# Kernel optimization log

Measured on AMD Instinct MI355X. Metric: run time of the kernel, lower is better.

The kernel has to match this reference:

```python
import jax, jax.numpy as jnp
import numpy as np

B, S = 256, 32          # sequence layout for the final (b, s, 1) reshape
BATCH = B * S           # 8192 flattened rows processed per call
IN, U, OUT = 32, 128, 1 # sensory inputs, interneurons, motor outputs
UNFOLDS = 6             # semi-implicit ODE solver unfolds


def _syn_sigmoid(v, mu, sigma):
    # v: [B, P]; mu, sigma: [P, Q] -> [B, P, Q] per-synapse gate
    return jax.nn.sigmoid(sigma * (v[:, :, None] - mu))


def setup_inputs() -> dict:
    key = jax.random.key(0)
    ks = jax.random.split(key, 12)
    inputs = jax.random.normal(ks[0], (BATCH, IN), dtype=jnp.float32)
    state = jax.random.normal(ks[1], (BATCH, U), dtype=jnp.float32)
    # adjacency in {-1, 0, 1} (wiring polarity), baked into W / erev as in _get_variables
    sens_adj = jax.random.randint(ks[2], (IN, U), -1, 2).astype(jnp.float32)
    adj = jax.random.randint(ks[3], (U, U), -1, 2).astype(jnp.float32)
    sensory_mu = jax.random.uniform(ks[4], (IN, U)) * 0.5 + 0.3
    sensory_sigma = jax.random.uniform(ks[5], (IN, U)) * 5.0 + 3.0
    # NOTE: original applies +w_init_min OUTSIDE the |adj| mask; reproduced faithfully
    sensory_W = jnp.abs(sens_adj) * jax.random.uniform(ks[6], (IN, U)) * 0.9 + 0.1
    sensory_erev = sens_adj  # erev_init_factor = 1
    mu = jax.random.uniform(ks[7], (U, U)) * 0.5 + 0.3
    sigma = jax.random.uniform(ks[8], (U, U)) * 5.0 + 3.0
    W = jnp.abs(adj) * jax.random.uniform(ks[9], (U, U)) * 0.9 + 0.1
    erev = adj
    vleak = jax.random.uniform(ks[10], (U,)) * 0.4 - 0.2
    gleak = jnp.ones((U,), jnp.float32)        # gleak_init_min == gleak_init_max == 1
    cm_t = jnp.ones((U,), jnp.float32) * 0.5    # cm_init_min == cm_init_max == 0.5
    in_w = jnp.ones((IN,), jnp.float32)         # affine input mapping (init ones/zeros)
    in_b = jnp.zeros((IN,), jnp.float32)
    out_w = jnp.ones((OUT,), jnp.float32)       # affine output mapping
    out_b = jnp.zeros((OUT,), jnp.float32)
    return dict(inputs=inputs, state=state, sensory_mu=sensory_mu,
                sensory_sigma=sensory_sigma, sensory_W=sensory_W,
                sensory_erev=sensory_erev, mu=mu, sigma=sigma, W=W, erev=erev,
                vleak=vleak, gleak=gleak, cm_t=cm_t, in_w=in_w, in_b=in_b,
                out_w=out_w, out_b=out_b, b=B, s=S)


def reference(inputs, state, sensory_mu, sensory_sigma, sensory_W, sensory_erev,
              mu, sigma, W, erev, vleak, gleak, cm_t, in_w, in_b, out_w, out_b,
              b, s):
    x = inputs * in_w + in_b                                   # _map_inputs (Affine)
    # sensory synapse activations, computed once: [BATCH, IN, U]
    sa = sensory_W * _syn_sigmoid(x, sensory_mu, sensory_sigma)
    w_num_s = jnp.sum(sa * sensory_erev, axis=1)               # [BATCH, U]
    w_den_s = jnp.sum(sa, axis=1)                              # [BATCH, U]

    def step(v, _):
        wa = W * _syn_sigmoid(v, mu, sigma)                    # [BATCH, U, U]
        w_num = jnp.sum(wa * erev, axis=1) + w_num_s
        w_den = jnp.sum(wa, axis=1) + w_den_s
        v_new = (cm_t * v + gleak * vleak + w_num) / (cm_t + gleak + w_den)
        return v_new, None

    v, _ = jax.lax.scan(step, state, None, length=UNFOLDS)
    outputs = (v[:, :OUT] * out_w + out_b).reshape(b, s, 1)    # _map_outputs
    return outputs, v
```

## Files before the change

### kernel.cpp

```cpp
#include <hip/hip_runtime.h>

#define NIN 32
#define NU  128
#define RPB 8
#define RPT 4
#define UNFOLDS 6
#define LOG2E 1.44269504088896340736f

typedef float float4v __attribute__((ext_vector_type(4)));

#define SPN (NIN * NU)
#define RPN (NU * NU)

__global__ void pack_params(const float* __restrict__ mu,
                            const float* __restrict__ sig,
                            const float* __restrict__ W,
                            const float* __restrict__ erev,
                            float4v* __restrict__ out, int n) {
    int idx = blockIdx.x * blockDim.x + threadIdx.x;
    if (idx < n) {
        float sg = sig[idx];
        float s2 = -LOG2E * sg;
        float sm2 = -s2 * mu[idx];
        float Wv = W[idx];
        float We = Wv * erev[idx];
        out[idx] = (float4v){s2, sm2, We, Wv};
    }
}

template <bool PACKED>
__global__ __launch_bounds__(256, 4)
void wormnet_main(const float* __restrict__ inputs,
                  const float* __restrict__ state,
                  const float4v* __restrict__ sp,
                  const float4v* __restrict__ rp,
                  const float* __restrict__ smu, const float* __restrict__ ssig,
                  const float* __restrict__ sW,  const float* __restrict__ serev,
                  const float* __restrict__ rmu, const float* __restrict__ rsig,
                  const float* __restrict__ rW,  const float* __restrict__ rerev,
                  const float* __restrict__ vleak,
                  const float* __restrict__ gleak,
                  const float* __restrict__ cm_t,
                  const float* __restrict__ in_w, const float* __restrict__ in_b,
                  const float* __restrict__ out_w, const float* __restrict__ out_b,
                  float* __restrict__ out_y,
                  float* __restrict__ out_v)
{
    __shared__ __align__(16) float xs[NIN * RPB];
    __shared__ __align__(16) float vs[2][NU * RPB];

    const int tid  = threadIdx.x;
    const int j    = tid & (NU - 1);
    const int rh   = tid >> 7;
    const int r0   = rh * RPT;
    const int base = blockIdx.x * RPB;

    {
        int i = tid & (NIN - 1);
        int r = tid >> 5;
        xs[i * RPB + r] = inputs[(base + r) * NIN + i] * in_w[i] + in_b[i];
    }
    {
        #pragma unroll
        for (int k = 0; k < 4; ++k) {
            int r = rh + 2 * k;
            vs[0][j * RPB + r] = state[(base + r) * NU + j];
        }
    }
    __syncthreads();

    float numS[RPT], denS[RPT];
    #pragma unroll
    for (int r = 0; r < RPT; ++r) { numS[r] = 0.0f; denS[r] = 0.0f; }

    #pragma unroll 4
    for (int i = 0; i < NIN; ++i) {
        float4v p;
        if (PACKED) {
            p = sp[i * NU + j];
        } else {
            int idx = i * NU + j;
            float sg = ssig[idx];
            float s2 = -LOG2E * sg;
            p = (float4v){s2, -s2 * smu[idx], sW[idx] * serev[idx], sW[idx]};
        }
        float4v xv = *(const float4v*)&xs[i * RPB + r0];
        #pragma unroll
        for (int r = 0; r < RPT; ++r) {
            float t = __builtin_fmaf(p.x, xv[r], p.y);
            float e = __builtin_amdgcn_exp2f(t);
            float sgm = __builtin_amdgcn_rcpf(1.0f + e);
            numS[r] = __builtin_fmaf(p.z, sgm, numS[r]);
            denS[r] = __builtin_fmaf(p.w, sgm, denS[r]);
        }
    }

    const float cm = cm_t[j];
    const float gl = gleak[j];
    const float glvl = gl * vleak[j];
    const float cg = cm + gl;
    float vold[RPT];
    #pragma unroll
    for (int r = 0; r < RPT; ++r) vold[r] = vs[0][j * RPB + r0 + r];

    int cur = 0;
    for (int u = 0; u < UNFOLDS; ++u) {
        float num[RPT], den[RPT];
        #pragma unroll
        for (int r = 0; r < RPT; ++r) { num[r] = numS[r]; den[r] = denS[r]; }

        #pragma unroll 4
        for (int i = 0; i < NU; ++i) {
            float4v p;
            if (PACKED) {
                p = rp[i * NU + j];
            } else {
                int idx = i * NU + j;
                float sg = rsig[idx];
                float s2 = -LOG2E * sg;
                p = (float4v){s2, -s2 * rmu[idx], rW[idx] * rerev[idx], rW[idx]};
            }
            float4v vv = *(const float4v*)&vs[cur][i * RPB + r0];
            #pragma unroll
            for (int r = 0; r < RPT; ++r) {
                float t = __builtin_fmaf(p.x, vv[r], p.y);
                float e = __builtin_amdgcn_exp2f(t);
                float sgm = __builtin_amdgcn_rcpf(1.0f + e);
                num[r] = __builtin_fmaf(p.z, sgm, num[r]);
                den[r] = __builtin_fmaf(p.w, sgm, den[r]);
            }
        }

        float4v vnew;
        #pragma unroll
        for (int r = 0; r < RPT; ++r) {
            float tn = __builtin_fmaf(cm, vold[r], glvl) + num[r];
            float td = cg + den[r];
            float vn = tn * __builtin_amdgcn_rcpf(td);
            vold[r] = vn;
            vnew[r] = vn;
        }
        *(float4v*)&vs[cur ^ 1][j * RPB + r0] = vnew;
        __syncthreads();
        cur ^= 1;
    }

    #pragma unroll
    for (int r = 0; r < RPT; ++r) {
        out_v[(base + r0 + r) * NU + j] = vold[r];
    }
    if (j == 0) {
        const float ow = out_w[0], ob = out_b[0];
        #pragma unroll
        for (int r = 0; r < RPT; ++r) {
            out_y[base + r0 + r] = __builtin_fmaf(vold[r], ow, ob);
        }
    }
}

extern "C" void kernel_launch(void* const* d_in, const int* in_sizes, int n_in,
                              void* d_out, int out_size, void* d_ws, size_t ws_size,
                              hipStream_t stream) {
    const float* inputs  = (const float*)d_in[0];
    const float* state   = (const float*)d_in[1];
    const float* smu     = (const float*)d_in[2];
    const float* ssig    = (const float*)d_in[3];
    const float* sW      = (const float*)d_in[4];
    const float* serev   = (const float*)d_in[5];
    const float* rmu     = (const float*)d_in[6];
    const float* rsig    = (const float*)d_in[7];
    const float* rW      = (const float*)d_in[8];
    const float* rerev   = (const float*)d_in[9];
    const float* vleak   = (const float*)d_in[10];
    const float* gleak   = (const float*)d_in[11];
    const float* cm_t    = (const float*)d_in[12];
    const float* in_w    = (const float*)d_in[13];
    const float* in_b    = (const float*)d_in[14];
    const float* out_w   = (const float*)d_in[15];
    const float* out_b   = (const float*)d_in[16];

    const int batch = in_sizes[1] / NU;
    float* out_y = (float*)d_out;
    float* out_v = (float*)d_out + batch;

    const size_t need = (size_t)(SPN + RPN) * sizeof(float4v);
    const bool packed = ws_size >= need;
    float4v* sp = (float4v*)d_ws;
    float4v* rp = sp + SPN;

    if (packed) {
        hipLaunchKernelGGL(pack_params, dim3((SPN + 255) / 256), dim3(256), 0, stream,
                           smu, ssig, sW, serev, sp, SPN);
        hipLaunchKernelGGL(pack_params, dim3((RPN + 255) / 256), dim3(256), 0, stream,
                           rmu, rsig, rW, rerev, rp, RPN);
    }

    dim3 grid(batch / RPB), block(256);
    if (packed) {
        hipLaunchKernelGGL((wormnet_main<true>), grid, block, 0, stream,
                           inputs, state, sp, rp,
                           smu, ssig, sW, serev, rmu, rsig, rW, rerev,
                           vleak, gleak, cm_t, in_w, in_b, out_w, out_b,
                           out_y, out_v);
    } else {
        hipLaunchKernelGGL((wormnet_main<false>), grid, block, 0, stream,
                           inputs, state, sp, rp,
                           smu, ssig, sW, serev, rmu, rsig, rW, rerev,
                           vleak, gleak, cm_t, in_w, in_b, out_w, out_b,
                           out_y, out_v);
    }
}
```

Measured before the change: 277.8 us.

## Double rows per thread and pair sigmoid reciprocals to halve rcp count

Each block now handles 16 rows and each thread 8 rows, so every packed parameter load is reused across twice as many batch rows. Sigmoids are computed in pairs: one reciprocal of the product of two denominators gives both values, trading a transcendental rcp for extra multiplies. The unpacked fallback path is removed, so the kernel now assumes the workspace is large enough. Occupancy is lowered to 2 blocks per CU to make room for the larger register footprint, and the grid is halved.

```diff
diff --git a/kernel.cpp b/kernel.cpp
--- a/kernel.cpp
+++ b/kernel.cpp
@@ -2,8 +2,8 @@
 
 #define NIN 32
 #define NU  128
-#define RPB 8
-#define RPT 4
+#define RPB 16
+#define RPT 8
 #define UNFOLDS 6
 #define LOG2E 1.44269504088896340736f
 
@@ -28,16 +28,11 @@
     }
 }
 
-template <bool PACKED>
-__global__ __launch_bounds__(256, 4)
+__global__ __launch_bounds__(256, 2)
 void wormnet_main(const float* __restrict__ inputs,
                   const float* __restrict__ state,
                   const float4v* __restrict__ sp,
                   const float4v* __restrict__ rp,
-                  const float* __restrict__ smu, const float* __restrict__ ssig,
-                  const float* __restrict__ sW,  const float* __restrict__ serev,
-                  const float* __restrict__ rmu, const float* __restrict__ rsig,
-                  const float* __restrict__ rW,  const float* __restrict__ rerev,
                   const float* __restrict__ vleak,
                   const float* __restrict__ gleak,
                   const float* __restrict__ cm_t,
@@ -58,13 +53,13 @@
     {
         int i = tid & (NIN - 1);
         int r = tid >> 5;
-        xs[i * RPB + r] = inputs[(base + r) * NIN + i] * in_w[i] + in_b[i];
+        xs[i * RPB + r]     = inputs[(base + r) * NIN + i] * in_w[i] + in_b[i];
+        xs[i * RPB + r + 8] = inputs[(base + r + 8) * NIN + i] * in_w[i] + in_b[i];
     }
     {
         #pragma unroll
-        for (int k = 0; k < 4; ++k) {
-            int r = rh + 2 * k;
-            vs[0][j * RPB + r] = state[(base + r) * NU + j];
+        for (int r = 0; r < RPT; ++r) {
+            vs[0][j * RPB + r0 + r] = state[(base + r0 + r) * NU + j];
         }
     }
     __syncthreads();
@@ -73,25 +68,29 @@
     #pragma unroll
     for (int r = 0; r < RPT; ++r) { numS[r] = 0.0f; denS[r] = 0.0f; }
 
-    #pragma unroll 4
-    for (int i = 0; i < NIN; ++i) {
-        float4v p;
-        if (PACKED) {
-            p = sp[i * NU + j];
-        } else {
-            int idx = i * NU + j;
-            float sg = ssig[idx];
-            float s2 = -LOG2E * sg;
-            p = (float4v){s2, -s2 * smu[idx], sW[idx] * serev[idx], sW[idx]};
-        }
-        float4v xv = *(const float4v*)&xs[i * RPB + r0];
-        #pragma unroll
-        for (int r = 0; r < RPT; ++r) {
-            float t = __builtin_fmaf(p.x, xv[r], p.y);
-            float e = __builtin_amdgcn_exp2f(t);
-            float sgm = __builtin_amdgcn_rcpf(1.0f + e);
-            numS[r] = __builtin_fmaf(p.z, sgm, numS[r]);
-            denS[r] = __builtin_fmaf(p.w, sgm, denS[r]);
+    {
+        const float4v* pp = sp + j;
+        #pragma unroll 2
+        for (int i = 0; i < NIN; ++i) {
+            float4v p = pp[0]; pp += NU;
+            float4v xa = *(const float4v*)&xs[i * RPB + r0];
+            float4v xb = *(const float4v*)&xs[i * RPB + r0 + 4];
+            float a[RPT];
+            #pragma unroll
+            for (int r = 0; r < 4; ++r) {
+                a[r]     = 1.0f + __builtin_amdgcn_exp2f(__builtin_fmaf(p.x, xa[r], p.y));
+                a[r + 4] = 1.0f + __builtin_amdgcn_exp2f(__builtin_fmaf(p.x, xb[r], p.y));
+            }
+            #pragma unroll
+            for (int q = 0; q < RPT / 2; ++q) {
+                float rq = __builtin_amdgcn_rcpf(a[2*q] * a[2*q+1]);
+                float s0 = rq * a[2*q+1];
+                float s1 = rq * a[2*q];
+                numS[2*q]   = __builtin_fmaf(p.z, s0, numS[2*q]);
+                denS[2*q]   = __builtin_fmaf(p.w, s0, denS[2*q]);
+                numS[2*q+1] = __builtin_fmaf(p.z, s1, numS[2*q+1]);
+                denS[2*q+1] = __builtin_fmaf(p.w, s1, denS[2*q+1]);
+            }
         }
     }
 
@@ -109,38 +108,38 @@
         #pragma unroll
         for (int r = 0; r < RPT; ++r) { num[r] = numS[r]; den[r] = denS[r]; }
 
-        #pragma unroll 4
+        const float4v* pp = rp + j;
+        #pragma unroll 2
         for (int i = 0; i < NU; ++i) {
-            float4v p;
-            if (PACKED) {
-                p = rp[i * NU + j];
-            } else {
-                int idx = i * NU + j;
-                float sg = rsig[idx];
-                float s2 = -LOG2E * sg;
-                p = (float4v){s2, -s2 * rmu[idx], rW[idx] * rerev[idx], rW[idx]};
+            float4v p = pp[0]; pp += NU;
+            float4v va = *(const float4v*)&vs[cur][i * RPB + r0];
+            float4v vb = *(const float4v*)&vs[cur][i * RPB + r0 + 4];
+            float a[RPT];
+            #pragma unroll
+            for (int r = 0; r < 4; ++r) {
+                a[r]     = 1.0f + __builtin_amdgcn_exp2f(__builtin_fmaf(p.x, va[r], p.y));
+                a[r + 4] = 1.0f + __builtin_amdgcn_exp2f(__builtin_fmaf(p.x, vb[r], p.y));
             }
-            float4v vv = *(const float4v*)&vs[cur][i * RPB + r0];
             #pragma unroll
-            for (int r = 0; r < RPT; ++r) {
-                float t = __builtin_fmaf(p.x, vv[r], p.y);
-                float e = __builtin_amdgcn_exp2f(t);
-                float sgm = __builtin_amdgcn_rcpf(1.0f + e);
-                num[r] = __builtin_fmaf(p.z, sgm, num[r]);
-                den[r] = __builtin_fmaf(p.w, sgm, den[r]);
+            for (int q = 0; q < RPT / 2; ++q) {
+                float rq = __builtin_amdgcn_rcpf(a[2*q] * a[2*q+1]);
+                float s0 = rq * a[2*q+1];
+                float s1 = rq * a[2*q];
+                num[2*q]   = __builtin_fmaf(p.z, s0, num[2*q]);
+                den[2*q]   = __builtin_fmaf(p.w, s0, den[2*q]);
+                num[2*q+1] = __builtin_fmaf(p.z, s1, num[2*q+1]);
+                den[2*q+1] = __builtin_fmaf(p.w, s1, den[2*q+1]);
             }
         }
 
-        float4v vnew;
         #pragma unroll
         for (int r = 0; r < RPT; ++r) {
             float tn = __builtin_fmaf(cm, vold[r], glvl) + num[r];
             float td = cg + den[r];
             float vn = tn * __builtin_amdgcn_rcpf(td);
             vold[r] = vn;
-            vnew[r] = vn;
+            vs[cur ^ 1][j * RPB + r0 + r] = vn;
         }
-        *(float4v*)&vs[cur ^ 1][j * RPB + r0] = vnew;
         __syncthreads();
         cur ^= 1;
     }
@@ -183,30 +182,17 @@
     float* out_y = (float*)d_out;
     float* out_v = (float*)d_out + batch;
 
-    const size_t need = (size_t)(SPN + RPN) * sizeof(float4v);
-    const bool packed = ws_size >= need;
     float4v* sp = (float4v*)d_ws;
     float4v* rp = sp + SPN;
 
-    if (packed) {
-        hipLaunchKernelGGL(pack_params, dim3((SPN + 255) / 256), dim3(256), 0, stream,
-                           smu, ssig, sW, serev, sp, SPN);
-        hipLaunchKernelGGL(pack_params, dim3((RPN + 255) / 256), dim3(256), 0, stream,
-                           rmu, rsig, rW, rerev, rp, RPN);
-    }
+    hipLaunchKernelGGL(pack_params, dim3((SPN + 255) / 256), dim3(256), 0, stream,
+                       smu, ssig, sW, serev, sp, SPN);
+    hipLaunchKernelGGL(pack_params, dim3((RPN + 255) / 256), dim3(256), 0, stream,
+                       rmu, rsig, rW, rerev, rp, RPN);
 
     dim3 grid(batch / RPB), block(256);
-    if (packed) {
-        hipLaunchKernelGGL((wormnet_main<true>), grid, block, 0, stream,
-                           inputs, state, sp, rp,
-                           smu, ssig, sW, serev, rmu, rsig, rW, rerev,
-                           vleak, gleak, cm_t, in_w, in_b, out_w, out_b,
-                           out_y, out_v);
-    } else {
-        hipLaunchKernelGGL((wormnet_main<false>), grid, block, 0, stream,
-                           inputs, state, sp, rp,
-                           smu, ssig, sW, serev, rmu, rsig, rW, rerev,
-                           vleak, gleak, cm_t, in_w, in_b, out_w, out_b,
-                           out_y, out_v);
-    }
+    hipLaunchKernelGGL(wormnet_main, grid, block, 0, stream,
+                       inputs, state, sp, rp,
+                       vleak, gleak, cm_t, in_w, in_b, out_w, out_b,
+                       out_y, out_v);
 }
```

Result: no change. 277.3 us (-0.2%).
